# Optimization experiments

Measured on AMD Instinct MI355X. Metric: run time of the kernel, lower is better.

Reference implementation:

```python
import jax, jax.numpy as jnp
import numpy as np

L = 880      # flattened RootMLP param count: (1*8+8) + (8*96+96)
HID = 8      # MLP hidden width
OUT = 96     # 2*data_size
DS = 48      # data_size
T = 64       # sequence length
BATCH = 4


def setup_inputs() -> dict:
    key = jax.random.key(0)
    k1, k2, k3, k4, k5 = jax.random.split(key, 5)
    xs = jax.random.normal(k1, (BATCH, T, DS), jnp.float32)
    ts = jax.random.uniform(k2, (BATCH, T), dtype=jnp.float32)
    theta0 = 0.1 * jax.random.normal(k3, (L,), jnp.float32)
    # near-identity A so matrix powers up to A^(T-1) stay bounded
    A = 0.99 * jnp.eye(L, dtype=jnp.float32) + (0.01 / np.sqrt(L)) * jax.random.normal(k4, (L, L), jnp.float32)
    B = 0.01 * jax.random.normal(k5, (L, DS), jnp.float32)
    return {"xs": xs, "ts": ts, "theta0": theta0, "A": A, "B": B, "aux": 0}


def _forward(xs, ts, theta0, A, B):
    Bt, T_, _ = xs.shape
    I = jnp.eye(L, dtype=A.dtype)

    # A_pows[t] = A^t for t = 0..T-1, via a cumulative matmul scan
    def step(P, _):
        return P @ A, P
    _, pows = jax.lax.scan(step, I, None, length=T_)  # (T, L, L)

    # K_conv = [B, A^0(A-I)B, ..., A^(T-3)(A-I)B]  -> (T-1, L, DS)
    M = (A - I) @ B
    K_tail = jnp.einsum('tij,jd->tid', pows[:T_ - 2], M)
    K_conv = jnp.concatenate([B[None], K_tail], axis=0)

    # FFT circular convolution of input signal with K_conv over time
    u = xs[:, 1:, :]                      # (B, T-1, DS)
    u_f = jnp.fft.fft(u, axis=1)
    K_f = jnp.fft.fft(K_conv, axis=0)     # (T-1, L, DS)
    thetas = jnp.fft.ifft(jnp.einsum('tld,btd->btl', K_f, u_f), axis=1).real

    # initial-condition convolution with K_conv0 = A^tau, tau = 0..T-2
    K0 = pows[:T_ - 1]                    # (T-1, L, L)
    sig = jnp.zeros((Bt, T_ - 1, L), xs.dtype)
    sig = sig.at[:, 0, :].set(theta0)
    sig = sig.at[:, 1, :].set(-(xs[:, 0, :] @ B.T))
    sig_f = jnp.fft.fft(sig, axis=1)
    K0_f = jnp.fft.fft(K0, axis=0)
    phi0 = jnp.fft.ifft(jnp.einsum('tlm,btm->btl', K0_f, sig_f), axis=1).real

    thetas = thetas + phi0
    thetas = jnp.concatenate([jnp.broadcast_to(theta0, (Bt, 1, L)), thetas], axis=1)  # (B, T, L)

    # apply RootMLP (1 -> HID -> OUT) with params unflattened from thetas
    W0 = thetas[..., :HID]                                    # (B,T,HID): W0 is (HID,1)
    b0 = thetas[..., HID:2 * HID]
    W1 = thetas[..., 2 * HID:2 * HID + OUT * HID].reshape(Bt, T_, OUT, HID)
    b1 = thetas[..., 2 * HID + OUT * HID:]
    h = jax.nn.relu(W0 * ts[..., None] + b0)                  # (B,T,HID)
    out = jnp.einsum('btoh,bth->bto', W1, h) + b1             # (B,T,OUT)
    # reconstruction head: tanh means, softplus stds
    return jnp.concatenate([jnp.tanh(out[..., :DS]), jax.nn.softplus(out[..., DS:])], axis=-1)


def reference(xs, ts, theta0, A, B, aux):
    return _forward(xs, ts, theta0, A, B)
```

## Files before the change

### kernel.cpp

```cpp
#include <hip/hip_runtime.h>
#include <math.h>

typedef unsigned int uint;
typedef unsigned short ushort;
typedef short s16x8 __attribute__((ext_vector_type(8)));
typedef float f32x4 __attribute__((ext_vector_type(4)));
typedef uint u32x4 __attribute__((ext_vector_type(4)));

#define L     880
#define LP    896
#define NC    64
#define WS    (NC * LP)
#define DS    48
#define OUTD  96
#define KCV   3072
#define NZ    3

#define OFF_E    0
#define OFF_WF   4415488
#define OFF_WB   (OFF_WF + 63 * WS)
#define OFF_KDT  (OFF_WB + 63 * WS / 2)
#define OFF_U    (OFF_KDT + LP * KCV / 2)
#define OFF_PART (OFF_U + 256 * KCV / 2)

__device__ inline ushort f2b(float f) {
  uint u = __builtin_bit_cast(uint, f);
  u += 0x7fffu + ((u >> 16) & 1u);
  return (ushort)(u >> 16);
}
__device__ inline float b2f(ushort b) {
  uint u = ((uint)b) << 16;
  return __builtin_bit_cast(float, u);
}

__global__ __launch_bounds__(256) void k_prepE(const float* __restrict__ A,
                                               ushort* __restrict__ EN,
                                               ushort* __restrict__ ET) {
  __shared__ float T[64][65];
  const int bi = blockIdx.y * 64, bj = blockIdx.x * 64;
  const int tid = threadIdx.x;
  const int r = tid >> 2, c0 = (tid & 3) * 16;
  const int gi = bi + r;
#pragma unroll
  for (int q = 0; q < 4; ++q) {
    int c = c0 + q * 4, gj = bj + c;
    float4 v = {0.f, 0.f, 0.f, 0.f};
    if (gi < L && gj < L) {
      v = *(const float4*)(A + gi * L + gj);
      if (gi == gj)     v.x -= 0.99f;
      if (gi == gj + 1) v.y -= 0.99f;
      if (gi == gj + 2) v.z -= 0.99f;
      if (gi == gj + 3) v.w -= 0.99f;
    }
    T[r][c] = v.x; T[r][c + 1] = v.y; T[r][c + 2] = v.z; T[r][c + 3] = v.w;
  }
  __syncthreads();
  {
    union { ushort s[16]; u32x4 v[2]; } pk;
#pragma unroll
    for (int i = 0; i < 16; ++i) pk.s[i] = f2b(T[r][c0 + i]);
    *(u32x4*)(EN + (size_t)(bi + r) * LP + bj + c0)     = pk.v[0];
    *(u32x4*)(EN + (size_t)(bi + r) * LP + bj + c0 + 8) = pk.v[1];
  }
  {
    union { ushort s[16]; u32x4 v[2]; } pk;
#pragma unroll
    for (int i = 0; i < 16; ++i) pk.s[i] = f2b(T[c0 + i][r]);
    *(u32x4*)(ET + (size_t)(bj + r) * LP + bi + c0)     = pk.v[0];
    *(u32x4*)(ET + (size_t)(bj + r) * LP + bi + c0 + 8) = pk.v[1];
  }
}

__global__ void k_prepW0(const float* __restrict__ B, const float* __restrict__ th0,
                         const float* __restrict__ xs, float* __restrict__ WF,
                         ushort* __restrict__ WB) {
  int idx = blockIdx.x * 256 + threadIdx.x;
  int c = idx / LP, l = idx % LP;
  float v = 0.f;
  if (l < L) {
    if (c < DS) v = B[l * DS + c];
    else if (c == DS) v = th0[l];
    else if (c < 53) {
      int b = c - 49;
      float s = 0.f;
      for (int d = 0; d < DS; ++d) s += B[l * DS + d] * xs[(b * 64) * DS + d];
      v = -s;
    }
  }
  WF[idx] = v;
  WB[idx] = f2b(v);
}

__global__ __launch_bounds__(256) void k_ladder(
    const ushort* __restrict__ sqA, const ushort* __restrict__ sqBT, float cs2,
    ushort* __restrict__ sqOutN, ushort* __restrict__ sqOutT, int ySq,
    const ushort* __restrict__ chA, const ushort* __restrict__ chBT, float csc,
    const float* __restrict__ chWFin, float* __restrict__ chWFout,
    ushort* __restrict__ chWBout) {
  __shared__ __align__(16) ushort As[2][64][72];
  __shared__ __align__(16) ushort Bs[2][64][72];
  const int tid = threadIdx.x;
  const bool isSq = (int)blockIdx.y < ySq;
  const int n0 = blockIdx.x * 64;
  const int m0 = isSq ? blockIdx.y * 64 : ((int)blockIdx.y - ySq) * 64;
  const ushort* Ab = isSq ? sqA : chA;
  const ushort* Bb = isSq ? sqBT : chBT;
  const int r = tid >> 2, kq = (tid & 3) * 16;
  const ushort* aptr = Ab + (size_t)(m0 + r) * LP + kq;
  const ushort* bptr = Bb + (size_t)(n0 + r) * LP + kq;
  const int wv = tid >> 6, lane = tid & 63;
  const int wm = (wv >> 1) * 32, wn = (wv & 1) * 32;
  const int lr = lane & 15, lg = lane >> 4;
  f32x4 acc[2][2] = {};
  u32x4 ra0 = *(const u32x4*)aptr;
  u32x4 ra1 = *(const u32x4*)(aptr + 8);
  u32x4 rb0 = *(const u32x4*)bptr;
  u32x4 rb1 = *(const u32x4*)(bptr + 8);
  const int kI = LP / 64;
  for (int it = 0; it < kI; ++it) {
    const int cur = it & 1;
    *(u32x4*)&As[cur][r][kq]     = ra0;
    *(u32x4*)&As[cur][r][kq + 8] = ra1;
    *(u32x4*)&Bs[cur][r][kq]     = rb0;
    *(u32x4*)&Bs[cur][r][kq + 8] = rb1;
    __syncthreads();
    if (it + 1 < kI) {
      ra0 = *(const u32x4*)(aptr + (it + 1) * 64);
      ra1 = *(const u32x4*)(aptr + (it + 1) * 64 + 8);
      rb0 = *(const u32x4*)(bptr + (it + 1) * 64);
      rb1 = *(const u32x4*)(bptr + (it + 1) * 64 + 8);
    }
#pragma unroll
    for (int ks = 0; ks < 2; ++ks) {
      s16x8 a0 = *(const s16x8*)&As[cur][wm + lr][ks * 32 + lg * 8];
      s16x8 a1 = *(const s16x8*)&As[cur][wm + 16 + lr][ks * 32 + lg * 8];
      s16x8 b0 = *(const s16x8*)&Bs[cur][wn + lr][ks * 32 + lg * 8];
      s16x8 b1 = *(const s16x8*)&Bs[cur][wn + 16 + lr][ks * 32 + lg * 8];
      acc[0][0] = __builtin_amdgcn_mfma_f32_16x16x32_bf16(a0, b0, acc[0][0], 0, 0, 0);
      acc[0][1] = __builtin_amdgcn_mfma_f32_16x16x32_bf16(a0, b1, acc[0][1], 0, 0, 0);
      acc[1][0] = __builtin_amdgcn_mfma_f32_16x16x32_bf16(a1, b0, acc[1][0], 0, 0, 0);
      acc[1][1] = __builtin_amdgcn_mfma_f32_16x16x32_bf16(a1, b1, acc[1][1], 0, 0, 0);
    }
  }
  if (isSq) {
    ushort (*T)[72] = As[0];
    __syncthreads();
#pragma unroll
    for (int fm = 0; fm < 2; ++fm)
#pragma unroll
      for (int fn = 0; fn < 2; ++fn)
#pragma unroll
        for (int rr = 0; rr < 4; ++rr) {
          int mi = wm + fm * 16 + lg * 4 + rr;
          int ni = wn + fn * 16 + lr;
          float v = acc[fm][fn][rr] + cs2 * b2f(sqA[(size_t)(m0 + mi) * LP + n0 + ni]);
          ushort bv = f2b(v);
          sqOutN[(size_t)(m0 + mi) * LP + n0 + ni] = bv;
          T[ni][mi] = bv;
        }
    if (sqOutT) {
      __syncthreads();
      int rt = tid >> 2, ct0 = (tid & 3) * 16;
      u32x4 o0 = *(const u32x4*)&T[rt][ct0];
      u32x4 o1 = *(const u32x4*)&T[rt][ct0 + 8];
      *(u32x4*)(sqOutT + (size_t)(n0 + rt) * LP + m0 + ct0)     = o0;
      *(u32x4*)(sqOutT + (size_t)(n0 + rt) * LP + m0 + ct0 + 8) = o1;
    }
  } else {
#pragma unroll
    for (int fm = 0; fm < 2; ++fm)
#pragma unroll
      for (int fn = 0; fn < 2; ++fn)
#pragma unroll
        for (int rr = 0; rr < 4; ++rr) {
          int m = m0 + wm + fm * 16 + lg * 4 + rr;
          int n = n0 + wn + fn * 16 + lr;
          float v = acc[fm][fn][rr] + csc * chWFin[(size_t)m * LP + n];
          chWFout[(size_t)m * LP + n] = v;
          chWBout[(size_t)m * LP + n] = f2b(v);
        }
  }
}

__global__ void k_kd(const float* __restrict__ WF, ushort* __restrict__ KDT) {
  __shared__ float D[48][65];
  const int j = blockIdx.x;
  const int l0 = blockIdx.y * 64;
  if (j < 63) {
    const float* Wj = WF + (size_t)j * WS;
    for (int e = threadIdx.x; e < 48 * 64; e += 256) {
      int d = e >> 6, ll = e & 63;
      float v = Wj[d * LP + l0 + ll];
      if (j > 0) v -= Wj[-(int)WS + d * LP + l0 + ll];
      D[d][ll] = v;
    }
  } else {
    for (int e = threadIdx.x; e < 48 * 64; e += 256) { int d = e >> 6, ll = e & 63; D[d][ll] = 0.f; }
  }
  __syncthreads();
  for (int e = threadIdx.x; e < 48 * 64; e += 256) {
    int ll = e / 48, d = e - ll * 48;
    KDT[(size_t)(l0 + ll) * KCV + j * 48 + d] = f2b(D[d][ll]);
  }
}

__global__ void k_u(const float* __restrict__ xs, ushort* __restrict__ U) {
  int idx = (blockIdx.x * 256 + threadIdx.x) * 4;
  int rr = idx / KCV, k = idx - rr * KCV;
  ushort4 v = {0, 0, 0, 0};
  if (rr < 252 && k < 3024) {
    int b = rr / 63, tau = rr - b * 63;
    int j = k / DS, d = k - j * DS;
    int s = tau - j; if (s < 0) s += 63;
    float4 x4 = *(const float4*)(xs + (size_t)(b * 64 + s + 1) * DS + d);
    v.x = f2b(x4.x); v.y = f2b(x4.y); v.z = f2b(x4.z); v.w = f2b(x4.w);
  }
  *(ushort4*)(U + idx) = v;
}

__global__ __launch_bounds__(256) void k_conv(const ushort* __restrict__ U,
                                              const ushort* __restrict__ KDT,
                                              float* __restrict__ part) {
  __shared__ __align__(16) ushort As[2][64][72];
  __shared__ __align__(16) ushort Bs[2][64][72];
  const int tid = threadIdx.x;
  const int n0 = blockIdx.x * 64, m0 = blockIdx.y * 64;
  const int kbase = blockIdx.z * (KCV / NZ);
  const int r = tid >> 2, kq = (tid & 3) * 16;
  const ushort* aptr = U + (size_t)(m0 + r) * KCV + kbase + kq;
  const ushort* bptr = KDT + (size_t)(n0 + r) * KCV + kbase + kq;
  const int wv = tid >> 6, lane = tid & 63;
  const int wm = (wv >> 1) * 32, wn = (wv & 1) * 32;
  const int lr = lane & 15, lg = lane >> 4;
  f32x4 acc[2][2] = {};
  u32x4 ra0 = *(const u32x4*)aptr;
  u32x4 ra1 = *(const u32x4*)(aptr + 8);
  u32x4 rb0 = *(const u32x4*)bptr;
  u32x4 rb1 = *(const u32x4*)(bptr + 8);
  const int kI = (KCV / NZ) / 64;
  for (int it = 0; it < kI; ++it) {
    const int cur = it & 1;
    *(u32x4*)&As[cur][r][kq]     = ra0;
    *(u32x4*)&As[cur][r][kq + 8] = ra1;
    *(u32x4*)&Bs[cur][r][kq]     = rb0;
    *(u32x4*)&Bs[cur][r][kq + 8] = rb1;
    __syncthreads();
    if (it + 1 < kI) {
      ra0 = *(const u32x4*)(aptr + (it + 1) * 64);
      ra1 = *(const u32x4*)(aptr + (it + 1) * 64 + 8);
      rb0 = *(const u32x4*)(bptr + (it + 1) * 64);
      rb1 = *(const u32x4*)(bptr + (it + 1) * 64 + 8);
    }
#pragma unroll
    for (int ks = 0; ks < 2; ++ks) {
      s16x8 a0 = *(const s16x8*)&As[cur][wm + lr][ks * 32 + lg * 8];
      s16x8 a1 = *(const s16x8*)&As[cur][wm + 16 + lr][ks * 32 + lg * 8];
      s16x8 b0 = *(const s16x8*)&Bs[cur][wn + lr][ks * 32 + lg * 8];
      s16x8 b1 = *(const s16x8*)&Bs[cur][wn + 16 + lr][ks * 32 + lg * 8];
      acc[0][0] = __builtin_amdgcn_mfma_f32_16x16x32_bf16(a0, b0, acc[0][0], 0, 0, 0);
      acc[0][1] = __builtin_amdgcn_mfma_f32_16x16x32_bf16(a0, b1, acc[0][1], 0, 0, 0);
      acc[1][0] = __builtin_amdgcn_mfma_f32_16x16x32_bf16(a1, b0, acc[1][0], 0, 0, 0);
      acc[1][1] = __builtin_amdgcn_mfma_f32_16x16x32_bf16(a1, b1, acc[1][1], 0, 0, 0);
    }
  }
  float* pp = part + (size_t)blockIdx.z * (256 * LP);
#pragma unroll
  for (int fm = 0; fm < 2; ++fm)
#pragma unroll
    for (int fn = 0; fn < 2; ++fn)
#pragma unroll
      for (int rr = 0; rr < 4; ++rr) {
        int m = m0 + wm + fm * 16 + lg * 4 + rr;
        int n = n0 + wn + fn * 16 + lr;
        pp[(size_t)m * LP + n] = acc[fm][fn][rr];
      }
}

__global__ __launch_bounds__(256) void k_final(const float* __restrict__ part,
                                               const float* __restrict__ WF,
                                               const float* __restrict__ th0,
                                               const float* __restrict__ ts,
                                               float* __restrict__ out) {
  __shared__ float th[LP];
  const int bt = blockIdx.x, b = bt >> 6, t = bt & 63;
  for (int l = threadIdx.x; l < LP; l += 256) {
    float v = 0.f;
    if (l < L) {
      if (t == 0) v = th0[l];
      else {
        int rr = b * 63 + (t - 1);
        v = part[(size_t)rr * LP + l]
          + part[(size_t)(256 * LP) + rr * LP + l]
          + part[(size_t)(2 * 256 * LP) + rr * LP + l];
        int tau = t - 1;
        v += WF[(size_t)tau * WS + DS * LP + l];
        int tw = (tau + 62) % 63;
        v += WF[(size_t)tw * WS + (49 + b) * LP + l];
      }
    }
    th[l] = v;
  }
  __syncthreads();
  int o = threadIdx.x;
  if (o < OUTD) {
    float tv = ts[bt];
    float acc = th[784 + o];
#pragma unroll
    for (int i = 0; i < 8; ++i) {
      float h = fmaxf(th[i] * tv + th[8 + i], 0.f);
      acc += th[16 + o * 8 + i] * h;
    }
    float rs;
    if (o < DS) rs = tanhf(acc);
    else        rs = fmaxf(acc, 0.f) + log1pf(expf(-fabsf(acc)));
    out[bt * OUTD + o] = rs;
  }
}

extern "C" void kernel_launch(void* const* d_in, const int* in_sizes, int n_in,
                              void* d_out, int out_size, void* d_ws, size_t ws_size,
                              hipStream_t stream) {
  const float* xs  = (const float*)d_in[0];
  const float* ts  = (const float*)d_in[1];
  const float* th0 = (const float*)d_in[2];
  const float* A   = (const float*)d_in[3];
  const float* B   = (const float*)d_in[4];
  float* out = (float*)d_out;
  float* ws  = (float*)d_ws;

  ushort* EP   = (ushort*)(ws + OFF_E);
  const size_t PL = (size_t)LP * LP;
  ushort* EN1  = EP + 0 * PL;
  ushort* ET1  = EP + 1 * PL;
  ushort* EN2  = EP + 2 * PL;
  ushort* ET2  = EP + 3 * PL;
  ushort* EN4  = EP + 4 * PL;
  ushort* ET4  = EP + 5 * PL;
  ushort* EN8  = EP + 6 * PL;
  ushort* ET8  = EP + 7 * PL;
  ushort* EN16 = EP + 8 * PL;
  ushort* ET16 = EP + 9 * PL;
  ushort* EN32 = EP + 10 * PL;
  float*  WF   = ws + OFF_WF;
  ushort* WB   = (ushort*)(ws + OFF_WB);
  ushort* KDT  = (ushort*)(ws + OFF_KDT);
  ushort* U    = (ushort*)(ws + OFF_U);
  float*  part = ws + OFF_PART;

  const float c1 = 0.99f;
  const float c2 = c1 * c1, c4 = c2 * c2, c8 = c4 * c4, c16 = c8 * c8, c32 = c16 * c16;

  k_prepE<<<dim3(14, 14), 256, 0, stream>>>(A, EN1, ET1);
  k_prepW0<<<(NC * LP) / 256, 256, 0, stream>>>(B, th0, xs, WF, WB);
  k_u<<<(256 * KCV / 4) / 256, 256, 0, stream>>>(xs, U);

  k_ladder<<<dim3(14, 15), 256, 0, stream>>>(EN1, ET1, 2.f * c1, EN2, ET2, 14,
                                             WB, EN1, c1, WF, WF + 1 * WS, WB + (size_t)1 * WS);
  k_ladder<<<dim3(14, 16), 256, 0, stream>>>(EN2, ET2, 2.f * c2, EN4, ET4, 14,
                                             WB, EN2, c2, WF, WF + 2 * WS, WB + (size_t)2 * WS);
  k_ladder<<<dim3(14, 18), 256, 0, stream>>>(EN4, ET4, 2.f * c4, EN8, ET8, 14,
                                             WB, EN4, c4, WF, WF + 4 * WS, WB + (size_t)4 * WS);
  k_ladder<<<dim3(14, 22), 256, 0, stream>>>(EN8, ET8, 2.f * c8, EN16, ET16, 14,
                                             WB, EN8, c8, WF, WF + 8 * WS, WB + (size_t)8 * WS);
  k_ladder<<<dim3(14, 30), 256, 0, stream>>>(EN16, ET16, 2.f * c16, EN32, nullptr, 14,
                                             WB, EN16, c16, WF, WF + 16 * WS, WB + (size_t)16 * WS);
  k_ladder<<<dim3(14, 31), 256, 0, stream>>>(nullptr, nullptr, 0.f, nullptr, nullptr, 0,
                                             WB, EN32, c32, WF, WF + 32 * WS, WB + (size_t)32 * WS);

  k_kd<<<dim3(64, 14), 256, 0, stream>>>(WF, KDT);
  k_conv<<<dim3(14, 4, NZ), 256, 0, stream>>>(U, KDT, part);
  k_final<<<256, 256, 0, stream>>>(part, WF, th0, ts, out);
}
```

Baseline: 110.7 us.

## Merge prep kernels, fuse KD build into last ladder step, split conv K further

Combines the three prep kernels into one launch. The first half of the KD-matrix construction is folded into the final ladder launch as extra blocks, so it runs alongside the chain GEMMs. The conv K-split rises from 3 to 6 to put more blocks in flight, and the final kernel sums the extra partial buffers. The GEMM core is moved into a shared helper that loads LDS fragments into registers before storing the next tile, and KDT reuses the E workspace region. This cuts launch count and adds parallelism, at the cost of more partial-sum traffic and a workspace aliasing risk.

```diff
diff --git a/kernel.cpp b/kernel.cpp
--- a/kernel.cpp
+++ b/kernel.cpp
@@ -10,17 +10,17 @@
 #define L     880
 #define LP    896
 #define NC    64
-#define WS    (NC * LP)
+#define WSZ   (NC * LP)
 #define DS    48
 #define OUTD  96
 #define KCV   3072
-#define NZ    3
+#define NZ    6
 
 #define OFF_E    0
+#define OFF_KDT  0
 #define OFF_WF   4415488
-#define OFF_WB   (OFF_WF + 63 * WS)
-#define OFF_KDT  (OFF_WB + 63 * WS / 2)
-#define OFF_U    (OFF_KDT + LP * KCV / 2)
+#define OFF_WB   (OFF_WF + 63 * WSZ)
+#define OFF_U    (OFF_WB + 63 * WSZ / 2)
 #define OFF_PART (OFF_U + 256 * KCV / 2)
 
 __device__ inline ushort f2b(float f) {
@@ -33,118 +33,195 @@
   return __builtin_bit_cast(float, u);
 }
 
-__global__ __launch_bounds__(256) void k_prepE(const float* __restrict__ A,
-                                               ushort* __restrict__ EN,
-                                               ushort* __restrict__ ET) {
-  __shared__ float T[64][65];
-  const int bi = blockIdx.y * 64, bj = blockIdx.x * 64;
+__device__ __forceinline__ void gemm64(const ushort* __restrict__ Ag,
+                                       const ushort* __restrict__ Bg,
+                                       int Kdim, int kIters, int kOff, int m0, int n0,
+                                       int tid, ushort (*As)[72], ushort (*Bs)[72],
+                                       f32x4 acc[2][2]) {
+  const int r = tid >> 2, kq = (tid & 3) * 16;
+  const ushort* aptr = Ag + (size_t)(m0 + r) * Kdim + kOff + kq;
+  const ushort* bptr = Bg + (size_t)(n0 + r) * Kdim + kOff + kq;
+  const int wv = tid >> 6, lane = tid & 63;
+  const int wm = (wv >> 1) * 32, wn = (wv & 1) * 32;
+  const int lr = lane & 15, lg = lane >> 4;
+  acc[0][0] = f32x4{0.f, 0.f, 0.f, 0.f};
+  acc[0][1] = f32x4{0.f, 0.f, 0.f, 0.f};
+  acc[1][0] = f32x4{0.f, 0.f, 0.f, 0.f};
+  acc[1][1] = f32x4{0.f, 0.f, 0.f, 0.f};
+  u32x4 ra0 = *(const u32x4*)aptr;
+  u32x4 ra1 = *(const u32x4*)(aptr + 8);
+  u32x4 rb0 = *(const u32x4*)bptr;
+  u32x4 rb1 = *(const u32x4*)(bptr + 8);
+  __syncthreads();
+  *(u32x4*)&As[r][kq]     = ra0;
+  *(u32x4*)&As[r][kq + 8] = ra1;
+  *(u32x4*)&Bs[r][kq]     = rb0;
+  *(u32x4*)&Bs[r][kq + 8] = rb1;
+  if (kIters > 1) {
+    ra0 = *(const u32x4*)(aptr + 64);
+    ra1 = *(const u32x4*)(aptr + 72);
+    rb0 = *(const u32x4*)(bptr + 64);
+    rb1 = *(const u32x4*)(bptr + 72);
+  }
+  __syncthreads();
+  for (int it = 0; it < kIters; ++it) {
+    const int cur = (it & 1) * 64, nxt = cur ^ 64;
+    s16x8 fa0[2], fa1[2], fb0[2], fb1[2];
+#pragma unroll
+    for (int k2 = 0; k2 < 2; ++k2) {
+      fa0[k2] = *(const s16x8*)&As[cur + wm + lr][k2 * 32 + lg * 8];
+      fa1[k2] = *(const s16x8*)&As[cur + wm + 16 + lr][k2 * 32 + lg * 8];
+      fb0[k2] = *(const s16x8*)&Bs[cur + wn + lr][k2 * 32 + lg * 8];
+      fb1[k2] = *(const s16x8*)&Bs[cur + wn + 16 + lr][k2 * 32 + lg * 8];
+    }
+    if (it + 1 < kIters) {
+      *(u32x4*)&As[nxt + r][kq]     = ra0;
+      *(u32x4*)&As[nxt + r][kq + 8] = ra1;
+      *(u32x4*)&Bs[nxt + r][kq]     = rb0;
+      *(u32x4*)&Bs[nxt + r][kq + 8] = rb1;
+      if (it + 2 < kIters) {
+        ra0 = *(const u32x4*)(aptr + (it + 2) * 64);
+        ra1 = *(const u32x4*)(aptr + (it + 2) * 64 + 8);
+        rb0 = *(const u32x4*)(bptr + (it + 2) * 64);
+        rb1 = *(const u32x4*)(bptr + (it + 2) * 64 + 8);
+      }
+    }
+#pragma unroll
+    for (int k2 = 0; k2 < 2; ++k2) {
+      acc[0][0] = __builtin_amdgcn_mfma_f32_16x16x32_bf16(fa0[k2], fb0[k2], acc[0][0], 0, 0, 0);
+      acc[0][1] = __builtin_amdgcn_mfma_f32_16x16x32_bf16(fa0[k2], fb1[k2], acc[0][1], 0, 0, 0);
+      acc[1][0] = __builtin_amdgcn_mfma_f32_16x16x32_bf16(fa1[k2], fb0[k2], acc[1][0], 0, 0, 0);
+      acc[1][1] = __builtin_amdgcn_mfma_f32_16x16x32_bf16(fa1[k2], fb1[k2], acc[1][1], 0, 0, 0);
+    }
+    __syncthreads();
+  }
+}
+
+__device__ __forceinline__ void kd_body(const float* __restrict__ WF, ushort* __restrict__ KDT,
+                                        int j, int l0, int tid, float (*D)[65]) {
+  __syncthreads();
+  if (j < 63) {
+    const float* Wj = WF + (size_t)j * WSZ;
+    for (int e = tid; e < 48 * 64; e += 256) {
+      int d = e >> 6, ll = e & 63;
+      float v = Wj[d * LP + l0 + ll];
+      if (j > 0) v -= Wj[-(int)WSZ + d * LP + l0 + ll];
+      D[d][ll] = v;
+    }
+  } else {
+    for (int e = tid; e < 48 * 64; e += 256) { int d = e >> 6, ll = e & 63; D[d][ll] = 0.f; }
+  }
+  __syncthreads();
+  for (int e = tid; e < 48 * 64; e += 256) {
+    int ll = e / 48, d = e - ll * 48;
+    KDT[(size_t)(l0 + ll) * KCV + j * 48 + d] = f2b(D[d][ll]);
+  }
+}
+
+__global__ __launch_bounds__(256) void k_prep(const float* __restrict__ A,
+                                              const float* __restrict__ B,
+                                              const float* __restrict__ th0,
+                                              const float* __restrict__ xs,
+                                              ushort* __restrict__ EN,
+                                              ushort* __restrict__ ET,
+                                              float* __restrict__ WF,
+                                              ushort* __restrict__ WB,
+                                              ushort* __restrict__ U) {
+  const int blk = blockIdx.x;
   const int tid = threadIdx.x;
-  const int r = tid >> 2, c0 = (tid & 3) * 16;
-  const int gi = bi + r;
-#pragma unroll
-  for (int q = 0; q < 4; ++q) {
-    int c = c0 + q * 4, gj = bj + c;
-    float4 v = {0.f, 0.f, 0.f, 0.f};
-    if (gi < L && gj < L) {
-      v = *(const float4*)(A + gi * L + gj);
+  if (blk < 196) {
+    __shared__ float T[64][65];
+    const int bi = (blk / 14) * 64, bj = (blk % 14) * 64;
+    const int r = tid >> 2, c0 = (tid & 3) * 16;
+    const int gi = bi + r;
+#pragma unroll
+    for (int q = 0; q < 4; ++q) {
+      int c = c0 + q * 4, gj = bj + c;
+      float4 v = {0.f, 0.f, 0.f, 0.f};
+      if (gi < L && gj + 3 < L) {
+        v = *(const float4*)(A + (size_t)gi * L + gj);
+      } else if (gi < L) {
+        if (gj + 0 < L) v.x = A[(size_t)gi * L + gj];
+        if (gj + 1 < L) v.y = A[(size_t)gi * L + gj + 1];
+        if (gj + 2 < L) v.z = A[(size_t)gi * L + gj + 2];
+        if (gj + 3 < L) v.w = A[(size_t)gi * L + gj + 3];
+      }
       if (gi == gj)     v.x -= 0.99f;
       if (gi == gj + 1) v.y -= 0.99f;
       if (gi == gj + 2) v.z -= 0.99f;
       if (gi == gj + 3) v.w -= 0.99f;
-    }
-    T[r][c] = v.x; T[r][c + 1] = v.y; T[r][c + 2] = v.z; T[r][c + 3] = v.w;
-  }
-  __syncthreads();
-  {
-    union { ushort s[16]; u32x4 v[2]; } pk;
-#pragma unroll
-    for (int i = 0; i < 16; ++i) pk.s[i] = f2b(T[r][c0 + i]);
-    *(u32x4*)(EN + (size_t)(bi + r) * LP + bj + c0)     = pk.v[0];
-    *(u32x4*)(EN + (size_t)(bi + r) * LP + bj + c0 + 8) = pk.v[1];
-  }
-  {
-    union { ushort s[16]; u32x4 v[2]; } pk;
-#pragma unroll
-    for (int i = 0; i < 16; ++i) pk.s[i] = f2b(T[c0 + i][r]);
-    *(u32x4*)(ET + (size_t)(bj + r) * LP + bi + c0)     = pk.v[0];
-    *(u32x4*)(ET + (size_t)(bj + r) * LP + bi + c0 + 8) = pk.v[1];
-  }
-}
-
-__global__ void k_prepW0(const float* __restrict__ B, const float* __restrict__ th0,
-                         const float* __restrict__ xs, float* __restrict__ WF,
-                         ushort* __restrict__ WB) {
-  int idx = blockIdx.x * 256 + threadIdx.x;
-  int c = idx / LP, l = idx % LP;
-  float v = 0.f;
-  if (l < L) {
-    if (c < DS) v = B[l * DS + c];
-    else if (c == DS) v = th0[l];
-    else if (c < 53) {
-      int b = c - 49;
-      float s = 0.f;
-      for (int d = 0; d < DS; ++d) s += B[l * DS + d] * xs[(b * 64) * DS + d];
-      v = -s;
-    }
-  }
-  WF[idx] = v;
-  WB[idx] = f2b(v);
+      T[r][c] = v.x; T[r][c + 1] = v.y; T[r][c + 2] = v.z; T[r][c + 3] = v.w;
+    }
+    __syncthreads();
+    {
+      union { ushort s[16]; u32x4 v[2]; } pk;
+#pragma unroll
+      for (int i = 0; i < 16; ++i) pk.s[i] = f2b(T[r][c0 + i]);
+      *(u32x4*)(EN + (size_t)(bi + r) * LP + bj + c0)     = pk.v[0];
+      *(u32x4*)(EN + (size_t)(bi + r) * LP + bj + c0 + 8) = pk.v[1];
+    }
+    {
+      union { ushort s[16]; u32x4 v[2]; } pk;
+#pragma unroll
+      for (int i = 0; i < 16; ++i) pk.s[i] = f2b(T[c0 + i][r]);
+      *(u32x4*)(ET + (size_t)(bj + r) * LP + bi + c0)     = pk.v[0];
+      *(u32x4*)(ET + (size_t)(bj + r) * LP + bi + c0 + 8) = pk.v[1];
+    }
+  } else if (blk < 210) {
+    int base = (blk - 196) * 4096;
+    for (int e = tid; e < 4096; e += 256) {
+      int idx = base + e;
+      int c = idx / LP, l = idx % LP;
+      float v = 0.f;
+      if (l < L) {
+        if (c < DS) v = B[l * DS + c];
+        else if (c == DS) v = th0[l];
+        else if (c < 53) {
+          int b = c - 49;
+          float s = 0.f;
+          for (int d = 0; d < DS; ++d) s += B[l * DS + d] * xs[(b * 64) * DS + d];
+          v = -s;
+        }
+      }
+      WF[idx] = v;
+      WB[idx] = f2b(v);
+    }
+  } else {
+    int idx = ((blk - 210) * 256 + tid) * 4;
+    int rr = idx / KCV, k = idx - rr * KCV;
+    ushort4 v = {0, 0, 0, 0};
+    if (rr < 252 && k < 3024) {
+      int b = rr / 63, tau = rr - b * 63;
+      int j = k / DS, d = k - j * DS;
+      int s = tau - j; if (s < 0) s += 63;
+      float4 x4 = *(const float4*)(xs + (size_t)(b * 64 + s + 1) * DS + d);
+      v.x = f2b(x4.x); v.y = f2b(x4.y); v.z = f2b(x4.z); v.w = f2b(x4.w);
+    }
+    *(ushort4*)(U + idx) = v;
+  }
 }
 
 __global__ __launch_bounds__(256) void k_ladder(
     const ushort* __restrict__ sqA, const ushort* __restrict__ sqBT, float cs2,
     ushort* __restrict__ sqOutN, ushort* __restrict__ sqOutT, int ySq,
-    const ushort* __restrict__ chA, const ushort* __restrict__ chBT, float csc,
-    const float* __restrict__ chWFin, float* __restrict__ chWFout,
-    ushort* __restrict__ chWBout) {
-  __shared__ __align__(16) ushort As[2][64][72];
-  __shared__ __align__(16) ushort Bs[2][64][72];
+    int nCh, const ushort* __restrict__ chWB, const ushort* __restrict__ chE, float csc,
+    const float* __restrict__ chWFsrc, float* __restrict__ chWFdst,
+    ushort* __restrict__ chWBdst,
+    int kdJ0, const float* __restrict__ kdWF, ushort* __restrict__ kdKDT) {
+  __shared__ __align__(16) ushort As[128][72];
+  __shared__ __align__(16) ushort Bs[128][72];
   const int tid = threadIdx.x;
-  const bool isSq = (int)blockIdx.y < ySq;
+  const int y = blockIdx.y;
   const int n0 = blockIdx.x * 64;
-  const int m0 = isSq ? blockIdx.y * 64 : ((int)blockIdx.y - ySq) * 64;
-  const ushort* Ab = isSq ? sqA : chA;
-  const ushort* Bb = isSq ? sqBT : chBT;
-  const int r = tid >> 2, kq = (tid & 3) * 16;
-  const ushort* aptr = Ab + (size_t)(m0 + r) * LP + kq;
-  const ushort* bptr = Bb + (size_t)(n0 + r) * LP + kq;
   const int wv = tid >> 6, lane = tid & 63;
   const int wm = (wv >> 1) * 32, wn = (wv & 1) * 32;
   const int lr = lane & 15, lg = lane >> 4;
-  f32x4 acc[2][2] = {};
-  u32x4 ra0 = *(const u32x4*)aptr;
-  u32x4 ra1 = *(const u32x4*)(aptr + 8);
-  u32x4 rb0 = *(const u32x4*)bptr;
-  u32x4 rb1 = *(const u32x4*)(bptr + 8);
-  const int kI = LP / 64;
-  for (int it = 0; it < kI; ++it) {
-    const int cur = it & 1;
-    *(u32x4*)&As[cur][r][kq]     = ra0;
-    *(u32x4*)&As[cur][r][kq + 8] = ra1;
-    *(u32x4*)&Bs[cur][r][kq]     = rb0;
-    *(u32x4*)&Bs[cur][r][kq + 8] = rb1;
-    __syncthreads();
-    if (it + 1 < kI) {
-      ra0 = *(const u32x4*)(aptr + (it + 1) * 64);
-      ra1 = *(const u32x4*)(aptr + (it + 1) * 64 + 8);
-      rb0 = *(const u32x4*)(bptr + (it + 1) * 64);
-      rb1 = *(const u32x4*)(bptr + (it + 1) * 64 + 8);
-    }
-#pragma unroll
-    for (int ks = 0; ks < 2; ++ks) {
-      s16x8 a0 = *(const s16x8*)&As[cur][wm + lr][ks * 32 + lg * 8];
-      s16x8 a1 = *(const s16x8*)&As[cur][wm + 16 + lr][ks * 32 + lg * 8];
-      s16x8 b0 = *(const s16x8*)&Bs[cur][wn + lr][ks * 32 + lg * 8];
-      s16x8 b1 = *(const s16x8*)&Bs[cur][wn + 16 + lr][ks * 32 + lg * 8];
-      acc[0][0] = __builtin_amdgcn_mfma_f32_16x16x32_bf16(a0, b0, acc[0][0], 0, 0, 0);
-      acc[0][1] = __builtin_amdgcn_mfma_f32_16x16x32_bf16(a0, b1, acc[0][1], 0, 0, 0);
-      acc[1][0] = __builtin_amdgcn_mfma_f32_16x16x32_bf16(a1, b0, acc[1][0], 0, 0, 0);
-      acc[1][1] = __builtin_amdgcn_mfma_f32_16x16x32_bf16(a1, b1, acc[1][1], 0, 0, 0);
-    }
-  }
-  if (isSq) {
-    ushort (*T)[72] = As[0];
-    __syncthreads();
+
+  if (y < ySq) {
+    const int m0 = y * 64;
+    f32x4 acc[2][2];
+    gemm64(sqA, sqBT, LP, LP / 64, 0, m0, n0, tid, As, Bs, acc);
+    ushort (*T)[72] = As;
 #pragma unroll
     for (int fm = 0; fm < 2; ++fm)
 #pragma unroll
@@ -160,109 +237,56 @@
         }
     if (sqOutT) {
       __syncthreads();
-      int rt = tid >> 2, ct0 = (tid & 3) * 16;
-      u32x4 o0 = *(const u32x4*)&T[rt][ct0];
-      u32x4 o1 = *(const u32x4*)&T[rt][ct0 + 8];
-      *(u32x4*)(sqOutT + (size_t)(n0 + rt) * LP + m0 + ct0)     = o0;
-      *(u32x4*)(sqOutT + (size_t)(n0 + rt) * LP + m0 + ct0 + 8) = o1;
-    }
+      const int nr = tid >> 2, ct0 = (tid & 3) * 16;
+      u32x4 o0 = *(const u32x4*)&T[nr][ct0];
+      u32x4 o1 = *(const u32x4*)&T[nr][ct0 + 8];
+      *(u32x4*)(sqOutT + (size_t)(n0 + nr) * LP + m0 + ct0)     = o0;
+      *(u32x4*)(sqOutT + (size_t)(n0 + nr) * LP + m0 + ct0 + 8) = o1;
+    }
+  } else if (y < ySq + nCh) {
+    const int t = y - ySq;
+    f32x4 acc[2][2];
+    gemm64(chWB + (size_t)t * WSZ, chE, LP, LP / 64, 0, 0, n0, tid, As, Bs, acc);
+    const float*  srcF = chWFsrc + (size_t)t * WSZ;
+    float*        dstF = chWFdst + (size_t)t * WSZ;
+    ushort*       dstB = chWBdst + (size_t)t * WSZ;
+#pragma unroll
+    for (int fm = 0; fm < 2; ++fm)
+#pragma unroll
+      for (int fn = 0; fn < 2; ++fn)
+#pragma unroll
+        for (int rr = 0; rr < 4; ++rr) {
+          int mi = wm + fm * 16 + lg * 4 + rr;
+          int ni = n0 + wn + fn * 16 + lr;
+          float v = acc[fm][fn][rr] + csc * srcF[(size_t)mi * LP + ni];
+          dstF[(size_t)mi * LP + ni] = v;
+          dstB[(size_t)mi * LP + ni] = f2b(v);
+        }
   } else {
-#pragma unroll
-    for (int fm = 0; fm < 2; ++fm)
-#pragma unroll
-      for (int fn = 0; fn < 2; ++fn)
-#pragma unroll
-        for (int rr = 0; rr < 4; ++rr) {
-          int m = m0 + wm + fm * 16 + lg * 4 + rr;
-          int n = n0 + wn + fn * 16 + lr;
-          float v = acc[fm][fn][rr] + csc * chWFin[(size_t)m * LP + n];
-          chWFout[(size_t)m * LP + n] = v;
-          chWBout[(size_t)m * LP + n] = f2b(v);
-        }
-  }
-}
-
-__global__ void k_kd(const float* __restrict__ WF, ushort* __restrict__ KDT) {
+    int j = kdJ0 + (y - ySq - nCh);
+    kd_body(kdWF, kdKDT, j, n0, tid, (float(*)[65])As);
+  }
+}
+
+__global__ __launch_bounds__(256) void k_kd(const float* __restrict__ WF,
+                                            ushort* __restrict__ KDT, int j0) {
   __shared__ float D[48][65];
-  const int j = blockIdx.x;
-  const int l0 = blockIdx.y * 64;
-  if (j < 63) {
-    const float* Wj = WF + (size_t)j * WS;
-    for (int e = threadIdx.x; e < 48 * 64; e += 256) {
-      int d = e >> 6, ll = e & 63;
-      float v = Wj[d * LP + l0 + ll];
-      if (j > 0) v -= Wj[-(int)WS + d * LP + l0 + ll];
-      D[d][ll] = v;
-    }
-  } else {
-    for (int e = threadIdx.x; e < 48 * 64; e += 256) { int d = e >> 6, ll = e & 63; D[d][ll] = 0.f; }
-  }
-  __syncthreads();
-  for (int e = threadIdx.x; e < 48 * 64; e += 256) {
-    int ll = e / 48, d = e - ll * 48;
-    KDT[(size_t)(l0 + ll) * KCV + j * 48 + d] = f2b(D[d][ll]);
-  }
-}
-
-__global__ void k_u(const float* __restrict__ xs, ushort* __restrict__ U) {
-  int idx = (blockIdx.x * 256 + threadIdx.x) * 4;
-  int rr = idx / KCV, k = idx - rr * KCV;
-  ushort4 v = {0, 0, 0, 0};
-  if (rr < 252 && k < 3024) {
-    int b = rr / 63, tau = rr - b * 63;
-    int j = k / DS, d = k - j * DS;
-    int s = tau - j; if (s < 0) s += 63;
-    float4 x4 = *(const float4*)(xs + (size_t)(b * 64 + s + 1) * DS + d);
-    v.x = f2b(x4.x); v.y = f2b(x4.y); v.z = f2b(x4.z); v.w = f2b(x4.w);
-  }
-  *(ushort4*)(U + idx) = v;
+  kd_body(WF, KDT, j0 + blockIdx.y, blockIdx.x * 64, threadIdx.x, D);
 }
 
 __global__ __launch_bounds__(256) void k_conv(const ushort* __restrict__ U,
                                               const ushort* __restrict__ KDT,
                                               float* __restrict__ part) {
-  __shared__ __align__(16) ushort As[2][64][72];
-  __shared__ __align__(16) ushort Bs[2][64][72];
+  __shared__ __align__(16) ushort As[128][72];
+  __shared__ __align__(16) ushort Bs[128][72];
   const int tid = threadIdx.x;
   const int n0 = blockIdx.x * 64, m0 = blockIdx.y * 64;
-  const int kbase = blockIdx.z * (KCV / NZ);
-  const int r = tid >> 2, kq = (tid & 3) * 16;
-  const ushort* aptr = U + (size_t)(m0 + r) * KCV + kbase + kq;
-  const ushort* bptr = KDT + (size_t)(n0 + r) * KCV + kbase + kq;
+  const int kOff = blockIdx.z * (KCV / NZ);
   const int wv = tid >> 6, lane = tid & 63;
   const int wm = (wv >> 1) * 32, wn = (wv & 1) * 32;
   const int lr = lane & 15, lg = lane >> 4;
-  f32x4 acc[2][2] = {};
-  u32x4 ra0 = *(const u32x4*)aptr;
-  u32x4 ra1 = *(const u32x4*)(aptr + 8);
-  u32x4 rb0 = *(const u32x4*)bptr;
-  u32x4 rb1 = *(const u32x4*)(bptr + 8);
-  const int kI = (KCV / NZ) / 64;
-  for (int it = 0; it < kI; ++it) {
-    const int cur = it & 1;
-    *(u32x4*)&As[cur][r][kq]     = ra0;
-    *(u32x4*)&As[cur][r][kq + 8] = ra1;
-    *(u32x4*)&Bs[cur][r][kq]     = rb0;
-    *(u32x4*)&Bs[cur][r][kq + 8] = rb1;
-    __syncthreads();
-    if (it + 1 < kI) {
-      ra0 = *(const u32x4*)(aptr + (it + 1) * 64);
-      ra1 = *(const u32x4*)(aptr + (it + 1) * 64 + 8);
-      rb0 = *(const u32x4*)(bptr + (it + 1) * 64);
-      rb1 = *(const u32x4*)(bptr + (it + 1) * 64 + 8);
-    }
-#pragma unroll
-    for (int ks = 0; ks < 2; ++ks) {
-      s16x8 a0 = *(const s16x8*)&As[cur][wm + lr][ks * 32 + lg * 8];
-      s16x8 a1 = *(const s16x8*)&As[cur][wm + 16 + lr][ks * 32 + lg * 8];
-      s16x8 b0 = *(const s16x8*)&Bs[cur][wn + lr][ks * 32 + lg * 8];
-      s16x8 b1 = *(const s16x8*)&Bs[cur][wn + 16 + lr][ks * 32 + lg * 8];
-      acc[0][0] = __builtin_amdgcn_mfma_f32_16x16x32_bf16(a0, b0, acc[0][0], 0, 0, 0);
-      acc[0][1] = __builtin_amdgcn_mfma_f32_16x16x32_bf16(a0, b1, acc[0][1], 0, 0, 0);
-      acc[1][0] = __builtin_amdgcn_mfma_f32_16x16x32_bf16(a1, b0, acc[1][0], 0, 0, 0);
-      acc[1][1] = __builtin_amdgcn_mfma_f32_16x16x32_bf16(a1, b1, acc[1][1], 0, 0, 0);
-    }
-  }
+  f32x4 acc[2][2];
+  gemm64(U, KDT, KCV, (KCV / NZ) / 64, kOff, m0, n0, tid, As, Bs, acc);
   float* pp = part + (size_t)blockIdx.z * (256 * LP);
 #pragma unroll
   for (int fm = 0; fm < 2; ++fm)
@@ -289,13 +313,13 @@
       if (t == 0) v = th0[l];
       else {
         int rr = b * 63 + (t - 1);
-        v = part[(size_t)rr * LP + l]
-          + part[(size_t)(256 * LP) + rr * LP + l]
-          + part[(size_t)(2 * 256 * LP) + rr * LP + l];
+        v = 0.f;
+#pragma unroll
+        for (int z = 0; z < NZ; ++z) v += part[(size_t)z * (256 * LP) + rr * LP + l];
         int tau = t - 1;
-        v += WF[(size_t)tau * WS + DS * LP + l];
+        v += WF[(size_t)tau * WSZ + DS * LP + l];
         int tw = (tau + 62) % 63;
-        v += WF[(size_t)tw * WS + (49 + b) * LP + l];
+        v += WF[(size_t)tw * WSZ + (49 + b) * LP + l];
       }
     }
     th[l] = v;
@@ -350,24 +374,28 @@
   const float c1 = 0.99f;
   const float c2 = c1 * c1, c4 = c2 * c2, c8 = c4 * c4, c16 = c8 * c8, c32 = c16 * c16;
 
-  k_prepE<<<dim3(14, 14), 256, 0, stream>>>(A, EN1, ET1);
-  k_prepW0<<<(NC * LP) / 256, 256, 0, stream>>>(B, th0, xs, WF, WB);
-  k_u<<<(256 * KCV / 4) / 256, 256, 0, stream>>>(xs, U);
+  k_prep<<<978, 256, 0, stream>>>(A, B, th0, xs, EN1, ET1, WF, WB, U);
 
   k_ladder<<<dim3(14, 15), 256, 0, stream>>>(EN1, ET1, 2.f * c1, EN2, ET2, 14,
-                                             WB, EN1, c1, WF, WF + 1 * WS, WB + (size_t)1 * WS);
+                                             1, WB, EN1, c1, WF, WF + 1 * WSZ, WB + (size_t)1 * WSZ,
+                                             0, nullptr, nullptr);
   k_ladder<<<dim3(14, 16), 256, 0, stream>>>(EN2, ET2, 2.f * c2, EN4, ET4, 14,
-                                             WB, EN2, c2, WF, WF + 2 * WS, WB + (size_t)2 * WS);
+                                             2, WB, EN2, c2, WF, WF + 2 * WSZ, WB + (size_t)2 * WSZ,
+                                             0, nullptr, nullptr);
   k_ladder<<<dim3(14, 18), 256, 0, stream>>>(EN4, ET4, 2.f * c4, EN8, ET8, 14,
-                                             WB, EN4, c4, WF, WF + 4 * WS, WB + (size_t)4 * WS);
+                                             4, WB, EN4, c4, WF, WF + 4 * WSZ, WB + (size_t)4 * WSZ,
+                                             0, nullptr, nullptr);
   k_ladder<<<dim3(14, 22), 256, 0, stream>>>(EN8, ET8, 2.f * c8, EN16, ET16, 14,
-                                             WB, EN8, c8, WF, WF + 8 * WS, WB + (size_t)8 * WS);
+                                             8, WB, EN8, c8, WF, WF + 8 * WSZ, WB + (size_t)8 * WSZ,
+                                             0, nullptr, nullptr);
   k_ladder<<<dim3(14, 30), 256, 0, stream>>>(EN16, ET16, 2.f * c16, EN32, nullptr, 14,
-                                             WB, EN16, c16, WF, WF + 16 * WS, WB + (size_t)16 * WS);
-  k_ladder<<<dim3(14, 31), 256, 0, stream>>>(nullptr, nullptr, 0.f, nullptr, nullptr, 0,
-                                             WB, EN32, c32, WF, WF + 32 * WS, WB + (size_t)32 * WS);
-
-  k_kd<<<dim3(64, 14), 256, 0, stream>>>(WF, KDT);
+                                             16, WB, EN16, c16, WF, WF + 16 * WSZ, WB + (size_t)16 * WSZ,
+                                             0, nullptr, nullptr);
+  k_ladder<<<dim3(14, 63), 256, 0, stream>>>(nullptr, nullptr, 0.f, nullptr, nullptr, 0,
+                                             31, WB, EN32, c32, WF, WF + 32 * WSZ, WB + (size_t)32 * WSZ,
+                                             0, WF, KDT);
+  k_kd<<<dim3(14, 32), 256, 0, stream>>>(WF, KDT, 32);
+
   k_conv<<<dim3(14, 4, NZ), 256, 0, stream>>>(U, KDT, part);
   k_final<<<256, 256, 0, stream>>>(part, WF, th0, ts, out);
 }
```

Result: no change. 112.7 us (+1.9%).
